# Performance work log

Hardware: AMD Instinct MI355X
Metric: run time of the kernel (lower is better)

The kernel has to match this reference:

```python
import jax, jax.numpy as jnp
import numpy as np

B, N, D_IN, D_OUT, H, ALPHA = 8, 2048, 128, 64, 1, 0.2


def setup_inputs() -> dict:
    key = jax.random.key(0)
    k1, k2, k3, k4 = jax.random.split(key, 4)
    x = jax.random.normal(k1, (B, N, D_IN), dtype=jnp.float32)
    adj = jax.random.randint(k2, (B, N, N), 0, 2, dtype=jnp.int32)
    # guarantee self-loops so no softmax row is entirely masked
    adj = jnp.maximum(adj, jnp.eye(N, dtype=jnp.int32)[None])
    # xavier_uniform with gain=1.414, as in the torch module
    lim_w = 1.414 * np.sqrt(6.0 / (D_IN + D_OUT * H))
    W = jax.random.uniform(k3, (D_OUT * H, D_IN), minval=-lim_w, maxval=lim_w, dtype=jnp.float32)
    b = jnp.zeros((D_OUT * H,), dtype=jnp.float32)
    lim_a = 1.414 * np.sqrt(6.0 / (H + 2 * D_OUT))
    a = jax.random.uniform(k4, (H, 2 * D_OUT), minval=-lim_a, maxval=lim_a, dtype=jnp.float32)
    return {"x": x, "adj_hat": adj, "W": W, "b": b, "a": a}


def reference(x, adj_hat, W, b, a):
    Bn, Nn = x.shape[:2]
    # projection: [B,N,d_in] -> [B,N,H,D]
    xp = (x @ W.T + b).reshape(Bn, Nn, H, D_OUT)
    # additive score a . [x_i ; x_j] split into two O(N) dot-products
    # (mathematically identical to the original O(N^2) concat formulation)
    a_src, a_dst = a[:, :D_OUT], a[:, D_OUT:]
    e_src = jnp.einsum('bnhd,hd->bnh', xp, a_src)  # score contribution of node i (query/p axis)
    e_dst = jnp.einsum('bnhd,hd->bnh', xp, a_dst)  # score contribution of node j (neighbor/q axis)
    e = e_src[:, :, None, :] + e_dst[:, None, :, :]  # [B,N,N,H]
    e = jax.nn.leaky_relu(e, ALPHA)
    e = jnp.where(adj_hat[..., None] == 0, -jnp.inf, e)
    att = jax.nn.softmax(e, axis=2)  # softmax over neighbor axis (torch dim=-2)
    res = jnp.einsum('bmnh,bnhd->bmhd', att, xp)  # weighted aggregation
    return res.reshape(Bn, Nn, H * D_OUT)  # concat_heads=True
```

## Files before the change

kernel.cpp:

```cpp
#include <hip/hip_runtime.h>
#include <hip/hip_bf16.h>
#include <cstdint>

#define NN 2048
#define BB 8
#define DIN 128
#define DOUT 64
#define PHN 256
#define NPH (NN / PHN)
#define PCH 130

typedef __attribute__((ext_vector_type(8))) short bf16x8;
typedef __attribute__((ext_vector_type(4))) float f32x4;

static __device__ __forceinline__ unsigned short f2b(float f) {
    union { __hip_bfloat16 h; unsigned short s; } u;
    u.h = __float2bfloat16(f);
    return u.s;
}

__global__ __launch_bounds__(256) void gat_xp_mfma(
    const float* __restrict__ x, const float* __restrict__ W,
    const float* __restrict__ bias, const float* __restrict__ a,
    unsigned short* __restrict__ xpT, float* __restrict__ e_src,
    float* __restrict__ e_dst)
{
    __shared__ float red[4 * 16 * 65];
    const int t = threadIdx.x;
    const int lane = t & 63;
    const int w = t >> 6;
    const int lr = lane & 15;
    const int g  = lane >> 4;
    const int r0 = blockIdx.x * 16;
    const int k0 = w * 32 + g * 8;

    const float* xr = x + (size_t)(r0 + lr) * DIN + k0;
    const float4 xa = *(const float4*)xr;
    const float4 xb4 = *(const float4*)(xr + 4);
    bf16x8 afr;
    afr[0]=f2b(xa.x);  afr[1]=f2b(xa.y);  afr[2]=f2b(xa.z);  afr[3]=f2b(xa.w);
    afr[4]=f2b(xb4.x); afr[5]=f2b(xb4.y); afr[6]=f2b(xb4.z); afr[7]=f2b(xb4.w);

    #pragma unroll
    for (int dt = 0; dt < 4; ++dt) {
        const float* wr = W + (size_t)(dt * 16 + lr) * DIN + k0;
        const float4 wa = *(const float4*)wr;
        const float4 wb = *(const float4*)(wr + 4);
        bf16x8 bfr;
        bfr[0]=f2b(wa.x); bfr[1]=f2b(wa.y); bfr[2]=f2b(wa.z); bfr[3]=f2b(wa.w);
        bfr[4]=f2b(wb.x); bfr[5]=f2b(wb.y); bfr[6]=f2b(wb.z); bfr[7]=f2b(wb.w);
        f32x4 acc = {0.f, 0.f, 0.f, 0.f};
        acc = __builtin_amdgcn_mfma_f32_16x16x32_bf16(afr, bfr, acc, 0, 0, 0);
        #pragma unroll
        for (int reg = 0; reg < 4; ++reg)
            red[w * 1040 + (g * 4 + reg) * 65 + dt * 16 + lr] = acc[reg];
    }
    __syncthreads();

    const int row = t >> 4;
    const int dq  = t & 15;
    const int b   = r0 >> 11;
    const int nb  = r0 & (NN - 1);
    float es = 0.f, ed = 0.f;
    #pragma unroll
    for (int j = 0; j < 4; ++j) {
        const int d = dq * 4 + j;
        const float v = red[0 * 1040 + row * 65 + d] + red[1 * 1040 + row * 65 + d]
                      + red[2 * 1040 + row * 65 + d] + red[3 * 1040 + row * 65 + d]
                      + bias[d];
        es += v * a[d];
        ed += v * a[DOUT + d];
        xpT[((size_t)(b * DOUT + d) << 11) + nb + row] = f2b(v);
    }
    es += __shfl_xor(es, 1); es += __shfl_xor(es, 2);
    es += __shfl_xor(es, 4); es += __shfl_xor(es, 8);
    ed += __shfl_xor(ed, 1); ed += __shfl_xor(ed, 2);
    ed += __shfl_xor(ed, 4); ed += __shfl_xor(ed, 8);
    if (dq == 0) {
        e_src[r0 + row] = es;
        e_dst[r0 + row] = ed;
    }
}

__global__ __launch_bounds__(256, 2) void gat_attn_mfma(
    const int* __restrict__ adj, const unsigned short* __restrict__ xpT,
    const float* __restrict__ e_src, const float* __restrict__ e_dst,
    float* __restrict__ out)
{
    __shared__ float d_lds[NN];
    __shared__ unsigned short p_lds[2][32 * PCH];
    __shared__ float mred[4];
    __shared__ float s_lds[16];
    __shared__ float bnd_lds[16];
    __shared__ float rs_lds[16];

    const int t = threadIdx.x;
    const int lane = t & 63;
    const int w = t >> 6;
    const int lr = lane & 15;
    const int g  = lane >> 4;
    const int b  = blockIdx.x >> 7;
    const int m0 = (blockIdx.x & 127) * 16;
    const size_t base = (size_t)b * NN;

    const int* aptr[4];
    #pragma unroll
    for (int it = 0; it < 4; ++it)
        aptr[it] = adj + ((base + (size_t)(m0 + it * 4 + w)) << 11) + lane * 4;

    int4 acur[4], amid[4], anew[4];
    #pragma unroll
    for (int it = 0; it < 4; ++it) acur[it] = *(const int4*)(aptr[it]);
    #pragma unroll
    for (int it = 0; it < 4; ++it) amid[it] = *(const int4*)(aptr[it] + PHN);

    float dm = -1e30f;
    #pragma unroll
    for (int i = 0; i < 8; ++i) {
        const float v = e_dst[base + i * 256 + t];
        d_lds[i * 256 + t] = v;
        dm = fmaxf(dm, v);
    }
    #pragma unroll
    for (int off = 32; off >= 1; off >>= 1) dm = fmaxf(dm, __shfl_xor(dm, off));
    if (lane == 0) mred[w] = dm;
    __syncthreads();
    const float dmax = fmaxf(fmaxf(mred[0], mred[1]), fmaxf(mred[2], mred[3]));
    if (t < 16) {
        const float s = e_src[base + m0 + t];
        const float e0 = s + dmax;
        s_lds[t] = s;
        bnd_lds[t] = fmaxf(e0, 0.2f * e0);
    }
    __syncthreads();

    float srow[4], brow[4];
    #pragma unroll
    for (int it = 0; it < 4; ++it) {
        srow[it] = s_lds[it * 4 + w];
        brow[it] = bnd_lds[it * 4 + w];
    }

    f32x4 acc = {0.f, 0.f, 0.f, 0.f};
    float rs_acc[4] = {0.f, 0.f, 0.f, 0.f};
    const unsigned short* xb = xpT + ((size_t)(b * DOUT + w * 16 + lr) << 11);

    const int c  = lane >> 1;
    const int jj = (lane & 1) * 4;

    for (int ph = 0; ph < NPH; ++ph) {
        const int nb0 = ph * PHN;

        bf16x8 bfr[8];
        #pragma unroll
        for (int ks = 0; ks < 8; ++ks)
            bfr[ks] = *(const bf16x8*)(xb + nb0 + ks * 32 + g * 8);

        if (ph + 2 < NPH) {
            #pragma unroll
            for (int it = 0; it < 4; ++it)
                anew[it] = *(const int4*)(aptr[it] + (ph + 2) * PHN);
        }

        const float4 dv = *(const float4*)(d_lds + nb0 + lane * 4);
        const float dvv[4] = {dv.x, dv.y, dv.z, dv.w};
        unsigned short* pb = &p_lds[ph & 1][0];
        #pragma unroll
        for (int it = 0; it < 4; ++it) {
            const int row = it * 4 + w;
            const float s = srow[it], bd = brow[it];
            const int av[4] = {acur[it].x, acur[it].y, acur[it].z, acur[it].w};
            float p[4];
            #pragma unroll
            for (int j = 0; j < 4; ++j) {
                const float e = s + dvv[j];
                const float le = fmaxf(e, 0.2f * e);
                const float pe = __expf(le - bd);
                p[j] = av[j] ? pe : 0.f;
            }
            rs_acc[it] += (p[0] + p[1]) + (p[2] + p[3]);
            unsigned int* pp32 = (unsigned int*)(pb + c * PCH + row * 8 + jj);
            pp32[0] = ((unsigned)f2b(p[1]) << 16) | f2b(p[0]);
            pp32[1] = ((unsigned)f2b(p[3]) << 16) | f2b(p[2]);
        }

        asm volatile("s_waitcnt lgkmcnt(0)" ::: "memory");
        __builtin_amdgcn_s_barrier();

        const unsigned int* pw = (const unsigned int*)pb;
        __builtin_amdgcn_s_setprio(1);
        #pragma unroll
        for (int ks = 0; ks < 8; ++ks) {
            const int wbase = (ks * 4 + g) * 65 + lr * 4;
            union { unsigned int u[4]; bf16x8 v; } af;
            af.u[0] = pw[wbase + 0];
            af.u[1] = pw[wbase + 1];
            af.u[2] = pw[wbase + 2];
            af.u[3] = pw[wbase + 3];
            acc = __builtin_amdgcn_mfma_f32_16x16x32_bf16(af.v, bfr[ks], acc, 0, 0, 0);
        }
        __builtin_amdgcn_s_setprio(0);

        #pragma unroll
        for (int it = 0; it < 4; ++it) { acur[it] = amid[it]; amid[it] = anew[it]; }
    }

    #pragma unroll
    for (int it = 0; it < 4; ++it) {
        float v = rs_acc[it];
        #pragma unroll
        for (int off = 32; off >= 1; off >>= 1) v += __shfl_xor(v, off);
        if (lane == 0) rs_lds[it * 4 + w] = v;
    }
    __syncthreads();

    #pragma unroll
    for (int reg = 0; reg < 4; ++reg) {
        const int row = g * 4 + reg;
        const float o = acc[reg] / rs_lds[row];
        out[(base + (size_t)(m0 + row)) * DOUT + w * 16 + lr] = o;
    }
}

extern "C" void kernel_launch(void* const* d_in, const int* in_sizes, int n_in,
                              void* d_out, int out_size, void* d_ws, size_t ws_size,
                              hipStream_t stream) {
    const float* x    = (const float*)d_in[0];
    const int*   adj  = (const int*)d_in[1];
    const float* W    = (const float*)d_in[2];
    const float* bvec = (const float*)d_in[3];
    const float* a    = (const float*)d_in[4];
    float* out = (float*)d_out;

    unsigned short* xpT = (unsigned short*)d_ws;
    float* e_src = (float*)((char*)d_ws + (1 << 21));
    float* e_dst = e_src + (size_t)BB * NN;

    gat_xp_mfma<<<(BB * NN) / 16, 256, 0, stream>>>(x, W, bvec, a, xpT, e_src, e_dst);
    gat_attn_mfma<<<BB * (NN / 16), 256, 0, stream>>>(adj, xpT, e_src, e_dst, out);
}
```

Before: 216.5 us.

## Pre-pack adjacency into bitmask and read bits from LDS in attention kernel

Adds a separate kernel that ballots the int32 adjacency matrix into 64-bit masks. The attention kernel then loads its 16 rows of mask bits into shared memory once and reads one bit per element, instead of streaming int4 adjacency registers through a three-stage prefetch. The aim is to shrink register pressure and memory traffic inside the attention loop, and the occupancy hint on launch bounds is dropped. The cost is that the full 128 MB adjacency is still read once by an extra kernel launch, plus a small mask write and reread.

```diff
diff --git a/kernel.cpp b/kernel.cpp
--- a/kernel.cpp
+++ b/kernel.cpp
@@ -17,6 +17,26 @@
     union { __hip_bfloat16 h; unsigned short s; } u;
     u.h = __float2bfloat16(f);
     return u.s;
+}
+
+__global__ __launch_bounds__(256) void gat_pack(
+    const int* __restrict__ adj, unsigned long long* __restrict__ mask64)
+{
+    const int wid  = (blockIdx.x * 256 + threadIdx.x) >> 6;
+    const int lane = threadIdx.x & 63;
+    const int c0 = wid * 32;
+    for (int i = 0; i < 32; ++i) {
+        const int c = c0 + i;
+        const int4 v = *(const int4*)(adj + ((size_t)c << 8) + lane * 4);
+        const unsigned long long m0 = __ballot(v.x != 0);
+        const unsigned long long m1 = __ballot(v.y != 0);
+        const unsigned long long m2 = __ballot(v.z != 0);
+        const unsigned long long m3 = __ballot(v.w != 0);
+        if (lane == 0) {
+            unsigned long long* o = mask64 + ((size_t)c << 2);
+            o[0] = m0; o[1] = m1; o[2] = m2; o[3] = m3;
+        }
+    }
 }
 
 __global__ __launch_bounds__(256) void gat_xp_mfma(
@@ -82,13 +102,14 @@
     }
 }
 
-__global__ __launch_bounds__(256, 2) void gat_attn_mfma(
-    const int* __restrict__ adj, const unsigned short* __restrict__ xpT,
+__global__ __launch_bounds__(256) void gat_attn_mfma(
+    const unsigned int* __restrict__ mask32, const unsigned short* __restrict__ xpT,
     const float* __restrict__ e_src, const float* __restrict__ e_dst,
     float* __restrict__ out)
 {
     __shared__ float d_lds[NN];
     __shared__ unsigned short p_lds[2][32 * PCH];
+    __shared__ unsigned int mk_lds[1024];
     __shared__ float mred[4];
     __shared__ float s_lds[16];
     __shared__ float bnd_lds[16];
@@ -103,16 +124,10 @@
     const int m0 = (blockIdx.x & 127) * 16;
     const size_t base = (size_t)b * NN;
 
-    const int* aptr[4];
-    #pragma unroll
-    for (int it = 0; it < 4; ++it)
-        aptr[it] = adj + ((base + (size_t)(m0 + it * 4 + w)) << 11) + lane * 4;
-
-    int4 acur[4], amid[4], anew[4];
-    #pragma unroll
-    for (int it = 0; it < 4; ++it) acur[it] = *(const int4*)(aptr[it]);
-    #pragma unroll
-    for (int it = 0; it < 4; ++it) amid[it] = *(const int4*)(aptr[it] + PHN);
+    {
+        const unsigned int* mbase = mask32 + (size_t)(b * NN + m0) * 64;
+        *(uint4*)&mk_lds[t * 4] = *(const uint4*)(mbase + t * 4);
+    }
 
     float dm = -1e30f;
     #pragma unroll
@@ -147,6 +162,8 @@
 
     const int c  = lane >> 1;
     const int jj = (lane & 1) * 4;
+    const int hi = lane >> 5;
+    const unsigned int sh = lane & 31;
 
     for (int ph = 0; ph < NPH; ++ph) {
         const int nb0 = ph * PHN;
@@ -155,12 +172,6 @@
         #pragma unroll
         for (int ks = 0; ks < 8; ++ks)
             bfr[ks] = *(const bf16x8*)(xb + nb0 + ks * 32 + g * 8);
-
-        if (ph + 2 < NPH) {
-            #pragma unroll
-            for (int it = 0; it < 4; ++it)
-                anew[it] = *(const int4*)(aptr[it] + (ph + 2) * PHN);
-        }
 
         const float4 dv = *(const float4*)(d_lds + nb0 + lane * 4);
         const float dvv[4] = {dv.x, dv.y, dv.z, dv.w};
@@ -169,14 +180,15 @@
         for (int it = 0; it < 4; ++it) {
             const int row = it * 4 + w;
             const float s = srow[it], bd = brow[it];
-            const int av[4] = {acur[it].x, acur[it].y, acur[it].z, acur[it].w};
+            const unsigned int* mrow = &mk_lds[row * 64 + ph * 8 + hi];
             float p[4];
             #pragma unroll
             for (int j = 0; j < 4; ++j) {
                 const float e = s + dvv[j];
                 const float le = fmaxf(e, 0.2f * e);
                 const float pe = __expf(le - bd);
-                p[j] = av[j] ? pe : 0.f;
+                const unsigned int bit = (mrow[j * 2] >> sh) & 1u;
+                p[j] = bit ? pe : 0.f;
             }
             rs_acc[it] += (p[0] + p[1]) + (p[2] + p[3]);
             unsigned int* pp32 = (unsigned int*)(pb + c * PCH + row * 8 + jj);
@@ -200,9 +212,6 @@
             acc = __builtin_amdgcn_mfma_f32_16x16x32_bf16(af.v, bfr[ks], acc, 0, 0, 0);
         }
         __builtin_amdgcn_s_setprio(0);
-
-        #pragma unroll
-        for (int it = 0; it < 4; ++it) { acur[it] = amid[it]; amid[it] = anew[it]; }
     }
 
     #pragma unroll
@@ -235,7 +244,11 @@
     unsigned short* xpT = (unsigned short*)d_ws;
     float* e_src = (float*)((char*)d_ws + (1 << 21));
     float* e_dst = e_src + (size_t)BB * NN;
-
+    unsigned long long* mask64 =
+        (unsigned long long*)((char*)d_ws + (4 << 20));
+
+    gat_pack<<<1024, 256, 0, stream>>>(adj, mask64);
     gat_xp_mfma<<<(BB * NN) / 16, 256, 0, stream>>>(x, W, bvec, a, xpT, e_src, e_dst);
-    gat_attn_mfma<<<BB * (NN / 16), 256, 0, stream>>>(adj, xpT, e_src, e_dst, out);
-}
+    gat_attn_mfma<<<BB * (NN / 16), 256, 0, stream>>>((const unsigned int*)mask64,
+                                                      xpT, e_src, e_dst, out);
+}
```

New measurement: 242.4 us. +12.0%, slower.
